# Optimization experiments

Measured on AMD Instinct MI355X. Metric: run time of the kernel, lower is better.

## Reference

```python
import jax, jax.numpy as jnp
import numpy as np

N_HOST, N_FLOW = 20000, 200000
D_HOST, D_FLOW, D_H, D_OUT, L = 64, 128, 256, 2, 2
E = 2000000


def _mean_agg(x_src, src, dst, num_dst):
    # SAGEConv default 'mean' neighbor aggregation: mean of source features per destination node.
    msg = x_src[src]                                            # [E, D]
    s = jax.ops.segment_sum(msg, dst, num_segments=num_dst)     # [num_dst, D]
    cnt = jax.ops.segment_sum(jnp.ones((src.shape[0],), x_src.dtype), dst, num_segments=num_dst)
    return s / jnp.maximum(cnt, 1.0)[:, None]


def setup_inputs() -> dict:
    key = jax.random.key(0)
    ks = jax.random.split(key, 20)
    s = 0.02
    inp = {
        'x_host': jax.random.normal(ks[0], (N_HOST, D_HOST), jnp.float32),
        'x_flow': jax.random.normal(ks[1], (N_FLOW, D_FLOW), jnp.float32),
        'eidx_hf_src': jax.random.randint(ks[2], (E,), 0, N_HOST, jnp.int32),
        'eidx_hf_dst': jax.random.randint(ks[3], (E,), 0, N_FLOW, jnp.int32),
        'eidx_fh_src': jax.random.randint(ks[4], (E,), 0, N_FLOW, jnp.int32),
        'eidx_fh_dst': jax.random.randint(ks[5], (E,), 0, N_HOST, jnp.int32),
        'host_proj_W': jax.random.normal(ks[6], (D_HOST, D_H), jnp.float32) * s,
        'host_proj_b': jnp.zeros((D_H,), jnp.float32),
        'flow_proj_W': jax.random.normal(ks[7], (D_FLOW, D_H), jnp.float32) * s,
        'flow_proj_b': jnp.zeros((D_H,), jnp.float32),
        # per-layer SAGEConv params: lin_l (neighbor agg, with bias), lin_r (root, no bias)
        'Wl_hf': jax.random.normal(ks[8], (L, D_H, D_H), jnp.float32) * s,
        'bl_hf': jnp.zeros((L, D_H), jnp.float32),
        'Wr_hf': jax.random.normal(ks[9], (L, D_H, D_H), jnp.float32) * s,
        'Wl_fh': jax.random.normal(ks[10], (L, D_H, D_H), jnp.float32) * s,
        'bl_fh': jnp.zeros((L, D_H), jnp.float32),
        'Wr_fh': jax.random.normal(ks[11], (L, D_H, D_H), jnp.float32) * s,
        'lin_W': jax.random.normal(ks[12], (D_H, D_OUT), jnp.float32) * s,
        'lin_b': jnp.zeros((D_OUT,), jnp.float32),
    }
    return inp


def reference(x_host, x_flow, eidx_hf_src, eidx_hf_dst, eidx_fh_src, eidx_fh_dst,
              host_proj_W, host_proj_b, flow_proj_W, flow_proj_b,
              Wl_hf, bl_hf, Wr_hf, Wl_fh, bl_fh, Wr_fh, lin_W, lin_b):
    n_host, n_flow = x_host.shape[0], x_flow.shape[0]
    h = jax.nn.relu(x_host @ host_proj_W + host_proj_b)   # [n_host, D_H]
    f = jax.nn.relu(x_flow @ flow_proj_W + flow_proj_b)   # [n_flow, D_H]
    for i in range(Wl_hf.shape[0]):
        # host -> flow SAGEConv
        agg_f = _mean_agg(h, eidx_hf_src, eidx_hf_dst, n_flow)
        new_f = agg_f @ Wl_hf[i] + bl_hf[i] + f @ Wr_hf[i]
        # flow -> host SAGEConv
        agg_h = _mean_agg(f, eidx_fh_src, eidx_fh_dst, n_host)
        new_h = agg_h @ Wl_fh[i] + bl_fh[i] + h @ Wr_fh[i]
        h = jax.nn.leaky_relu(new_h, 0.01)
        f = jax.nn.leaky_relu(new_f, 0.01)
    return f @ lin_W + lin_b  # logits for flow nodes [n_flow, D_OUT]
```

## Files before the change

### kernel.cpp

```cpp
#include <hip/hip_runtime.h>

#define NH    20000
#define NF    200000
#define DHOST 64
#define DFLOW 128
#define DHID  256
#define NE    2000000
#define NLAYER 2

typedef __attribute__((ext_vector_type(8))) short s16x8;
typedef __attribute__((ext_vector_type(4))) float f32x4;

__device__ __forceinline__ unsigned short f2bf(float x) {
    unsigned u = __builtin_bit_cast(unsigned, x);
    unsigned r = (u + 0x7fffu + ((u >> 16) & 1u)) >> 16;
    return (unsigned short)r;
}
__device__ __forceinline__ float bf2f(unsigned short h) {
    unsigned u = ((unsigned)h) << 16;
    return __builtin_bit_cast(float, u);
}

typedef const __attribute__((address_space(1))) unsigned int guint;
typedef __attribute__((address_space(3))) unsigned int luint;
__device__ __forceinline__ void gld16(const void* g, void* l) {
    __builtin_amdgcn_global_load_lds((guint*)g, (luint*)l, 16, 0, 0);
}

__device__ __forceinline__ void dq8(uint2 u, float s, float* a) {
#pragma unroll
    for (int j = 0; j < 4; ++j) {
        a[j]     += s * (float)((signed char)(u.x >> (8 * j)));
        a[4 + j] += s * (float)((signed char)(u.y >> (8 * j)));
    }
}

__global__ void zero_k(int* __restrict__ p, int n) {
    int i = blockIdx.x * 256 + threadIdx.x;
    if (i < n) p[i] = 0;
}

__global__ __launch_bounds__(256) void tpose_k(const float* __restrict__ W, unsigned short* __restrict__ Wt, int K) {
    __shared__ float T[32][33];
    int bx = blockIdx.x, by = blockIdx.y;
    const float* Wz = W + (size_t)blockIdx.z * K * 256;
    unsigned short* Wtz = Wt + (size_t)blockIdx.z * K * 256;
    int tx = threadIdx.x & 31, ty = threadIdx.x >> 5;
#pragma unroll
    for (int i = 0; i < 4; ++i) {
        int k = by * 32 + ty + i * 8;
        T[ty + i * 8][tx] = Wz[(size_t)k * 256 + bx * 32 + tx];
    }
    __syncthreads();
#pragma unroll
    for (int i = 0; i < 4; ++i) {
        int n = bx * 32 + ty + i * 8;
        Wtz[(size_t)n * K + by * 32 + tx] = f2bf(T[tx][ty + i * 8]);
    }
}

__global__ void scan1_k(const int* __restrict__ in, int n, int* __restrict__ out, int* __restrict__ bsum) {
    __shared__ int wsum[4];
    int t = threadIdx.x;
    int lane = t & 63, wave = t >> 6;
    int idx = blockIdx.x * 1024 + t * 4;
    int v[4]; int s = 0;
#pragma unroll
    for (int i = 0; i < 4; ++i) { v[i] = (idx + i < n) ? in[idx + i] : 0; s += v[i]; }
    int inc = s;
#pragma unroll
    for (int off = 1; off < 64; off <<= 1) { int u = __shfl_up(inc, off); if (lane >= off) inc += u; }
    if (lane == 63) wsum[wave] = inc;
    __syncthreads();
    int woff = 0;
    for (int w = 0; w < wave; ++w) woff += wsum[w];
    int ex = woff + inc - s;
#pragma unroll
    for (int i = 0; i < 4; ++i) { if (idx + i < n) out[idx + i] = ex; ex += v[i]; }
    if (t == 255) bsum[blockIdx.x] = woff + inc;
}

__global__ __launch_bounds__(256) void histAB(const int* __restrict__ dstA, const int* __restrict__ dstB,
                                              int E, int* __restrict__ gbhA, int* __restrict__ gbhB) {
    __shared__ int lh[391];
    const int g = blockIdx.y;
    const int* dst = g ? dstB : dstA;
    int* gbh = g ? gbhB : gbhA;
    const int SH = g ? 6 : 9;
    const int NBKT = g ? 313 : 391;
    for (int b = threadIdx.x; b < NBKT; b += 256) lh[b] = 0;
    __syncthreads();
#pragma unroll
    for (int k = 0; k < 8; ++k) {
        int i = blockIdx.x * 2048 + k * 256 + threadIdx.x;
        if (i < E) atomicAdd(&lh[dst[i] >> SH], 1);
    }
    __syncthreads();
    for (int b = threadIdx.x; b < NBKT; b += 256) if (lh[b]) atomicAdd(&gbh[b], lh[b]);
}

__global__ void initcur_k(int* __restrict__ bko, int* __restrict__ gcur, int nbkt, int E) {
    int i = blockIdx.x * 256 + threadIdx.x;
    if (i < nbkt) gcur[i] = bko[i];
    if (i == nbkt) bko[nbkt] = E;
}

__global__ __launch_bounds__(256) void binpassAB(const int* __restrict__ srcA, const int* __restrict__ dstA,
                                                 const int* __restrict__ srcB, const int* __restrict__ dstB,
                                                 int E, int* __restrict__ gcurA, int* __restrict__ gcurB,
                                                 int* __restrict__ pairsA, int* __restrict__ pairsB) {
    __shared__ int lh[391], resv[391], lc[391];
    const int g = blockIdx.y;
    const int* src = g ? srcB : srcA;
    const int* dst = g ? dstB : dstA;
    int* gcur = g ? gcurB : gcurA;
    int* pairs = g ? pairsB : pairsA;
    const int SH = g ? 6 : 9;
    const int NBKT = g ? 313 : 391;
    const int MSK = (1 << SH) - 1;
    const int tid = threadIdx.x;
    const int e0 = blockIdx.x * 8192;
    for (int b = tid; b < NBKT; b += 256) { lh[b] = 0; lc[b] = 0; }
    __syncthreads();
#pragma unroll 4
    for (int k = 0; k < 32; ++k) {
        int i = e0 + k * 256 + tid;
        if (i < E) atomicAdd(&lh[dst[i] >> SH], 1);
    }
    __syncthreads();
    for (int b = tid; b < NBKT; b += 256) if (lh[b]) resv[b] = atomicAdd(&gcur[b], lh[b]);
    __syncthreads();
#pragma unroll 4
    for (int k = 0; k < 32; ++k) {
        int i = e0 + k * 256 + tid;
        if (i < E) {
            int d = dst[i];
            int b = d >> SH;
            int p = resv[b] + atomicAdd(&lc[b], 1);
            pairs[p] = src[i] | ((d & MSK) << 18);
        }
    }
}

__global__ __launch_bounds__(256) void csrfinAB(const int* __restrict__ pairsA, const int* __restrict__ bkoA,
                                                const int* __restrict__ pairsB, const int* __restrict__ bkoB,
                                                int NBA, int E,
                                                int* __restrict__ rpA, int* __restrict__ colA,
                                                int* __restrict__ rpB, int* __restrict__ colB) {
    __shared__ int cnt[512], pos[512];
    __shared__ int wsum[4];
    const int tid = threadIdx.x;
    const bool isA = (int)blockIdx.x < NBA;
    const int b = isA ? blockIdx.x : blockIdx.x - NBA;
    const int SH = isA ? 9 : 6;
    const int NPB = isA ? 512 : 64;
    const int N = isA ? NF : NH;
    const int* pairs = isA ? pairsA : pairsB;
    const int* bko = isA ? bkoA : bkoB;
    int* rowptr = isA ? rpA : rpB;
    int* col = isA ? colA : colB;
    const int nb = b << SH;
    const int beg = bko[b], end = bko[b + 1];
    for (int i = tid; i < NPB; i += 256) cnt[i] = 0;
    __syncthreads();
    for (int i = beg + tid; i < end; i += 256) atomicAdd(&cnt[pairs[i] >> 18], 1);
    __syncthreads();
    int lane = tid & 63, wave = tid >> 6;
    if (NPB == 512) {
        int a = cnt[2 * tid], b2 = cnt[2 * tid + 1];
        int s = a + b2, incl = s;
#pragma unroll
        for (int off = 1; off < 64; off <<= 1) { int u = __shfl_up(incl, off); if (lane >= off) incl += u; }
        if (lane == 63) wsum[wave] = incl;
        __syncthreads();
        int woff = 0;
        for (int w = 0; w < wave; ++w) woff += wsum[w];
        int ex = woff + incl - s;
        pos[2 * tid] = ex; pos[2 * tid + 1] = ex + a;
    } else {
        if (tid < NPB) {
            int a = cnt[tid], incl = a;
#pragma unroll
            for (int off = 1; off < 64; off <<= 1) { int u = __shfl_up(incl, off); if (lane >= off) incl += u; }
            pos[tid] = incl - a;
        }
    }
    __syncthreads();
    for (int i = tid; i < NPB; i += 256) {
        int node = nb + i;
        if (node < N) rowptr[node] = beg + pos[i];
    }
    if (tid == 0 && end == E) rowptr[N] = E;
    __syncthreads();
    for (int i = beg + tid; i < end; i += 256) {
        int pk = pairs[i];
        int p = atomicAdd(&pos[pk >> 18], 1);
        col[beg + p] = pk & 0x3FFFF;
    }
}

__global__ __launch_bounds__(256) void agg8_q8(const signed char* __restrict__ qf,
                                               const float* __restrict__ scl,
                                               const int* __restrict__ rowptr,
                                               const int* __restrict__ col,
                                               unsigned short* __restrict__ outp, int n) {
    int w = (blockIdx.x << 2) + (threadIdx.x >> 6);
    if (w >= n) return;
    int lane = threadIdx.x & 63;
    int half = lane >> 5, l5 = lane & 31;
    int beg = rowptr[w], end = rowptr[w + 1];
    int T = end - beg;
    const signed char* base = qf + l5 * 8;
    float a0[8], a1[8], a2[8], a3[8], a4[8], a5[8], a6[8], a7[8];
#pragma unroll
    for (int j = 0; j < 8; ++j) {
        a0[j] = 0.f; a1[j] = 0.f; a2[j] = 0.f; a3[j] = 0.f;
        a4[j] = 0.f; a5[j] = 0.f; a6[j] = 0.f; a7[j] = 0.f;
    }
    int i = beg;
    int nb16 = T >> 4;
    {
        const int* cp = col + beg + half * 8;
        for (int k = 0; k < nb16; ++k) {
            int c0 = cp[k * 16 + 0], c1 = cp[k * 16 + 1], c2 = cp[k * 16 + 2], c3 = cp[k * 16 + 3];
            int c4 = cp[k * 16 + 4], c5 = cp[k * 16 + 5], c6 = cp[k * 16 + 6], c7 = cp[k * 16 + 7];
            uint2 u0 = *reinterpret_cast<const uint2*>(base + (size_t)c0 * DHID);
            uint2 u1 = *reinterpret_cast<const uint2*>(base + (size_t)c1 * DHID);
            uint2 u2 = *reinterpret_cast<const uint2*>(base + (size_t)c2 * DHID);
            uint2 u3 = *reinterpret_cast<const uint2*>(base + (size_t)c3 * DHID);
            uint2 u4 = *reinterpret_cast<const uint2*>(base + (size_t)c4 * DHID);
            uint2 u5 = *reinterpret_cast<const uint2*>(base + (size_t)c5 * DHID);
            uint2 u6 = *reinterpret_cast<const uint2*>(base + (size_t)c6 * DHID);
            uint2 u7 = *reinterpret_cast<const uint2*>(base + (size_t)c7 * DHID);
            float s0 = scl[c0], s1 = scl[c1], s2 = scl[c2], s3 = scl[c3];
            float s4 = scl[c4], s5 = scl[c5], s6 = scl[c6], s7 = scl[c7];
            dq8(u0, s0, a0); dq8(u1, s1, a1); dq8(u2, s2, a2); dq8(u3, s3, a3);
            dq8(u4, s4, a4); dq8(u5, s5, a5); dq8(u6, s6, a6); dq8(u7, s7, a7);
        }
    }
    i += nb16 * 16;
    if (end - i >= 8) {
        const int* cp = col + i + half * 4;
        int c0 = cp[0], c1 = cp[1], c2 = cp[2], c3 = cp[3];
        uint2 u0 = *reinterpret_cast<const uint2*>(base + (size_t)c0 * DHID);
        uint2 u1 = *reinterpret_cast<const uint2*>(base + (size_t)c1 * DHID);
        uint2 u2 = *reinterpret_cast<const uint2*>(base + (size_t)c2 * DHID);
        uint2 u3 = *reinterpret_cast<const uint2*>(base + (size_t)c3 * DHID);
        float s0 = scl[c0], s1 = scl[c1], s2 = scl[c2], s3 = scl[c3];
        dq8(u0, s0, a0); dq8(u1, s1, a1); dq8(u2, s2, a2); dq8(u3, s3, a3);
        i += 8;
    }
    for (int e = i + half; e < end; e += 2) {
        int c = col[e];
        uint2 u = *reinterpret_cast<const uint2*>(base + (size_t)c * DHID);
        dq8(u, scl[c], a0);
    }
    int deg = T > 0 ? T : 1;
    float inv = 1.0f / (float)deg;
    s16x8 o;
#pragma unroll
    for (int j = 0; j < 8; ++j) {
        float s = ((a0[j] + a1[j]) + (a2[j] + a3[j])) + ((a4[j] + a5[j]) + (a6[j] + a7[j]));
        s += __shfl_xor(s, 32);
        o[j] = (short)f2bf(s * inv);
    }
    if (half == 0)
        *reinterpret_cast<s16x8*>(outp + (size_t)w * DHID + l5 * 8) = o;
}

__device__ __forceinline__ unsigned swz(unsigned r, unsigned cb) {
    return r * 128u + (cb ^ ((r & 7u) << 4));
}

union SmU {
    struct { char A[64 * 128]; char B[256 * 128]; } st;
    unsigned short tile[64][256];
};

__device__ __forceinline__ void pass64(const unsigned short* A, const unsigned short* Wt,
                                       int m0, int M, int lane, int wave, int wr, int wc,
                                       f32x4 (&acc)[2][4], SmU& sm) {
    for (int k0 = 0; k0 < DHID; k0 += 64) {
        __syncthreads();
        {
            int r = wave * 8 + (lane >> 3);
            int gr = m0 + r; if (gr >= M) gr = M - 1;
            int gs = (lane & 7) ^ (r & 7);
            gld16(A + (size_t)gr * DHID + k0 + gs * 8, sm.st.A + wave * 1024);
        }
#pragma unroll
        for (int i = 0; i < 4; ++i) {
            int u = wave * 4 + i;
            int nn = u * 8 + (lane >> 3);
            int gs = (lane & 7) ^ (nn & 7);
            gld16(Wt + (size_t)nn * DHID + k0 + gs * 8, sm.st.B + u * 1024);
        }
        __syncthreads();
#pragma unroll
        for (int kk = 0; kk < 2; ++kk) {
            s16x8 ar[2], br[4];
            unsigned colb = (unsigned)(kk * 64 + (lane >> 4) * 16);
#pragma unroll
            for (int mf = 0; mf < 2; ++mf)
                ar[mf] = *reinterpret_cast<const s16x8*>(sm.st.A + swz((unsigned)(wr * 32 + mf * 16 + (lane & 15)), colb));
#pragma unroll
            for (int nf = 0; nf < 4; ++nf)
                br[nf] = *reinterpret_cast<const s16x8*>(sm.st.B + swz((unsigned)(wc * 64 + nf * 16 + (lane & 15)), colb));
#pragma unroll
            for (int mf = 0; mf < 2; ++mf)
#pragma unroll
                for (int nf = 0; nf < 4; ++nf)
                    acc[mf][nf] = __builtin_amdgcn_mfma_f32_16x16x32_bf16(ar[mf], br[nf], acc[mf][nf], 0, 0, 0);
        }
    }
}

template<int ACT, int POST>
__device__ __forceinline__ void epi64(f32x4 (&acc)[2][4], const float* bias, SmU& sm,
                                      int m0, int M, int lane, int wave, int wr, int wc,
                                      unsigned short* outp, signed char* q, float* scl) {
    const int col0 = wc * 64 + (lane & 15);
    float bc[4];
#pragma unroll
    for (int nf = 0; nf < 4; ++nf) bc[nf] = bias[col0 + nf * 16];
    if (POST == 0) {
#pragma unroll
        for (int mf = 0; mf < 2; ++mf) {
            int row = m0 + wr * 32 + mf * 16 + (lane >> 4) * 4;
#pragma unroll
            for (int j = 0; j < 4; ++j) {
                if (row + j < M) {
#pragma unroll
                    for (int nf = 0; nf < 4; ++nf) {
                        float v = acc[mf][nf][j] + bc[nf];
                        if (ACT == 1) v = fmaxf(v, 0.0f);
                        else if (ACT == 2) v = v > 0.0f ? v : 0.01f * v;
                        outp[(size_t)(row + j) * DHID + col0 + nf * 16] = f2bf(v);
                    }
                }
            }
        }
        return;
    }
    __syncthreads();
#pragma unroll
    for (int mf = 0; mf < 2; ++mf) {
        int rl = wr * 32 + mf * 16 + (lane >> 4) * 4;
#pragma unroll
        for (int j = 0; j < 4; ++j)
#pragma unroll
            for (int nf = 0; nf < 4; ++nf) {
                float v = acc[mf][nf][j] + bc[nf];
                if (ACT == 1) v = fmaxf(v, 0.0f);
                else if (ACT == 2) v = v > 0.0f ? v : 0.01f * v;
                sm.tile[rl + j][col0 + nf * 16] = f2bf(v);
            }
    }
    __syncthreads();
    const int half = lane >> 5, l5 = lane & 31;
    for (int t = 0; t < 4; ++t) {
        int local = wave * 8 + half * 4 + t;
        int node = m0 + local;
        s16x8 tr = *reinterpret_cast<const s16x8*>(&sm.tile[local][l5 * 8]);
        float v[8]; float m = 0.0f;
#pragma unroll
        for (int j = 0; j < 8; ++j) { v[j] = bf2f((unsigned short)tr[j]); m = fmaxf(m, fabsf(v[j])); }
#pragma unroll
        for (int off = 1; off < 32; off <<= 1) m = fmaxf(m, __shfl_xor(m, off));
        if (node < M) {
            if (POST == 1)
                *reinterpret_cast<s16x8*>(outp + (size_t)node * DHID + l5 * 8) = tr;
            float si = (m > 0.0f) ? 127.0f / m : 0.0f;
            if (l5 == 0) scl[node] = m * (1.0f / 127.0f);
            uint2 pk;
            pk.x = ((unsigned)((int)__builtin_rintf(v[0] * si) & 255))
                 | ((unsigned)((int)__builtin_rintf(v[1] * si) & 255) << 8)
                 | ((unsigned)((int)__builtin_rintf(v[2] * si) & 255) << 16)
                 | ((unsigned)((int)__builtin_rintf(v[3] * si) & 255) << 24);
            pk.y = ((unsigned)((int)__builtin_rintf(v[4] * si) & 255))
                 | ((unsigned)((int)__builtin_rintf(v[5] * si) & 255) << 8)
                 | ((unsigned)((int)__builtin_rintf(v[6] * si) & 255) << 16)
                 | ((unsigned)((int)__builtin_rintf(v[7] * si) & 255) << 24);
            *reinterpret_cast<uint2*>(q + (size_t)node * DHID + l5 * 8) = pk;
        }
    }
}

template<int ACT, int FUSE, int POST>
__global__ __launch_bounds__(512) void mgemm64(const unsigned short* A1, const unsigned short* W1t,
                                               const float* __restrict__ bias,
                                               const unsigned short* A2, const unsigned short* W2t,
                                               unsigned short* outp, signed char* q, float* scl, int M) {
    __shared__ SmU sm;
    const int tid = threadIdx.x;
    const int lane = tid & 63, wave = tid >> 6;
    const int wr = wave >> 2, wc = wave & 3;
    const int m0 = blockIdx.x * 64;
    f32x4 acc[2][4];
#pragma unroll
    for (int a = 0; a < 2; ++a)
#pragma unroll
        for (int b = 0; b < 4; ++b) acc[a][b] = (f32x4)0.0f;
    pass64(A1, W1t, m0, M, lane, wave, wr, wc, acc, sm);
    if (FUSE) pass64(A2, W2t, m0, M, lane, wave, wr, wc, acc, sm);
    epi64<ACT, POST>(acc, bias, sm, m0, M, lane, wave, wr, wc, outp, q, scl);
}

template<int K1, int ACT, int POST>
__global__ __launch_bounds__(512) void mgemm64_f32(const float* __restrict__ A1, const unsigned short* W1t,
                                                   const float* __restrict__ bias,
                                                   unsigned short* outp, signed char* q, float* scl, int M) {
    __shared__ SmU sm;
    const int tid = threadIdx.x;
    const int lane = tid & 63, wave = tid >> 6;
    const int wr = wave >> 2, wc = wave & 3;
    const int m0 = blockIdx.x * 64;
    f32x4 acc[2][4];
#pragma unroll
    for (int a = 0; a < 2; ++a)
#pragma unroll
        for (int b = 0; b < 4; ++b) acc[a][b] = (f32x4)0.0f;

    for (int k0 = 0; k0 < K1; k0 += 64) {
        __syncthreads();
        {
            int r = tid >> 3, gc = tid & 7;
            int gr = m0 + r; if (gr >= M) gr = M - 1;
            const float* src = A1 + (size_t)gr * K1 + k0 + gc * 8;
            float4 v0 = *reinterpret_cast<const float4*>(src);
            float4 v1 = *reinterpret_cast<const float4*>(src + 4);
            s16x8 o;
            o[0] = (short)f2bf(v0.x); o[1] = (short)f2bf(v0.y);
            o[2] = (short)f2bf(v0.z); o[3] = (short)f2bf(v0.w);
            o[4] = (short)f2bf(v1.x); o[5] = (short)f2bf(v1.y);
            o[6] = (short)f2bf(v1.z); o[7] = (short)f2bf(v1.w);
            *reinterpret_cast<s16x8*>(sm.st.A + swz((unsigned)r, (unsigned)(gc * 16))) = o;
        }
#pragma unroll
        for (int i = 0; i < 4; ++i) {
            int u = wave * 4 + i;
            int nn = u * 8 + (lane >> 3);
            int gs = (lane & 7) ^ (nn & 7);
            gld16(W1t + (size_t)nn * K1 + k0 + gs * 8, sm.st.B + u * 1024);
        }
        __syncthreads();
#pragma unroll
        for (int kk = 0; kk < 2; ++kk) {
            s16x8 ar[2], br[4];
            unsigned colb = (unsigned)(kk * 64 + (lane >> 4) * 16);
#pragma unroll
            for (int mf = 0; mf < 2; ++mf)
                ar[mf] = *reinterpret_cast<const s16x8*>(sm.st.A + swz((unsigned)(wr * 32 + mf * 16 + (lane & 15)), colb));
#pragma unroll
            for (int nf = 0; nf < 4; ++nf)
                br[nf] = *reinterpret_cast<const s16x8*>(sm.st.B + swz((unsigned)(wc * 64 + nf * 16 + (lane & 15)), colb));
#pragma unroll
            for (int mf = 0; mf < 2; ++mf)
#pragma unroll
                for (int nf = 0; nf < 4; ++nf)
                    acc[mf][nf] = __builtin_amdgcn_mfma_f32_16x16x32_bf16(ar[mf], br[nf], acc[mf][nf], 0, 0, 0);
        }
    }
    epi64<ACT, POST>(acc, bias, sm, m0, M, lane, wave, wr, wc, outp, q, scl);
}

template<int QOUT>
__global__ __launch_bounds__(512) void mgemm_faq(const unsigned short* Fin, const unsigned short* Wrt,
                                                 const float* __restrict__ bias,
                                                 const signed char* __restrict__ Hq,
                                                 const float* __restrict__ sclH,
                                                 const int* __restrict__ rowptr,
                                                 const int* __restrict__ colv,
                                                 unsigned short* Fout,
                                                 signed char* __restrict__ Fq,
                                                 float* __restrict__ sclF, int M) {
    __shared__ SmU sm;
    const int tid = threadIdx.x;
    const int lane = tid & 63, wave = tid >> 6;
    const int wr = wave >> 2, wc = wave & 3;
    const int m0 = blockIdx.x * 64;
    f32x4 acc[2][4];
#pragma unroll
    for (int a = 0; a < 2; ++a)
#pragma unroll
        for (int b = 0; b < 4; ++b) acc[a][b] = (f32x4)0.0f;

    pass64(Fin, Wrt, m0, M, lane, wave, wr, wc, acc, sm);
    __syncthreads();

    const int col0 = wc * 64 + (lane & 15);
    float bc[4];
#pragma unroll
    for (int nf = 0; nf < 4; ++nf) bc[nf] = bias[col0 + nf * 16];
#pragma unroll
    for (int mf = 0; mf < 2; ++mf) {
        int rl = wr * 32 + mf * 16 + (lane >> 4) * 4;
#pragma unroll
        for (int j = 0; j < 4; ++j)
#pragma unroll
            for (int nf = 0; nf < 4; ++nf)
                sm.tile[rl + j][col0 + nf * 16] = f2bf(acc[mf][nf][j] + bc[nf]);
    }
    __syncthreads();

    const int half = lane >> 5, l5 = lane & 31;
    const signed char* base = Hq + l5 * 8;
    for (int t = 0; t < 8; ++t) {
        int local = wave * 8 + t;
        int node = m0 + local;
        if (node >= M) break;
        int beg = rowptr[node], end = rowptr[node + 1];
        int T = end - beg;
        int nb8 = T >> 3;
        float a0[8], a1[8], a2[8], a3[8];
#pragma unroll
        for (int j = 0; j < 8; ++j) { a0[j] = 0.f; a1[j] = 0.f; a2[j] = 0.f; a3[j] = 0.f; }
        const int* cp = colv + beg + half * 4;
        for (int k = 0; k < nb8; ++k) {
            int c0 = cp[k * 8 + 0], c1 = cp[k * 8 + 1], c2 = cp[k * 8 + 2], c3 = cp[k * 8 + 3];
            uint2 u0 = *reinterpret_cast<const uint2*>(base + (size_t)c0 * DHID);
            uint2 u1 = *reinterpret_cast<const uint2*>(base + (size_t)c1 * DHID);
            uint2 u2 = *reinterpret_cast<const uint2*>(base + (size_t)c2 * DHID);
            uint2 u3 = *reinterpret_cast<const uint2*>(base + (size_t)c3 * DHID);
            float s0 = sclH[c0], s1 = sclH[c1], s2 = sclH[c2], s3 = sclH[c3];
            dq8(u0, s0, a0); dq8(u1, s1, a1); dq8(u2, s2, a2); dq8(u3, s3, a3);
        }
        for (int i = beg + nb8 * 8 + half; i < end; i += 2) {
            int c = colv[i];
            uint2 u = *reinterpret_cast<const uint2*>(base + (size_t)c * DHID);
            dq8(u, sclH[c], a0);
        }
        float inv = 1.0f / (float)(T > 0 ? T : 1);
        s16x8 tr = *reinterpret_cast<const s16x8*>(&sm.tile[local][l5 * 8]);
        float v[8]; float m = 0.0f;
        s16x8 o;
#pragma unroll
        for (int j = 0; j < 8; ++j) {
            float s = (a0[j] + a1[j]) + (a2[j] + a3[j]);
            s += __shfl_xor(s, 32);
            float x = bf2f((unsigned short)tr[j]) + s * inv;
            x = x > 0.0f ? x : 0.01f * x;
            v[j] = x; o[j] = (short)f2bf(x);
            m = fmaxf(m, fabsf(x));
        }
        if (half == 0)
            *reinterpret_cast<s16x8*>(Fout + (size_t)node * DHID + l5 * 8) = o;
        if (QOUT) {
#pragma unroll
            for (int off = 1; off < 32; off <<= 1) m = fmaxf(m, __shfl_xor(m, off));
            float si = (m > 0.0f) ? 127.0f / m : 0.0f;
            if (half == 0 && l5 == 0) sclF[node] = m * (1.0f / 127.0f);
            if (half == 0) {
                uint2 pk;
                pk.x = ((unsigned)((int)__builtin_rintf(v[0] * si) & 255))
                     | ((unsigned)((int)__builtin_rintf(v[1] * si) & 255) << 8)
                     | ((unsigned)((int)__builtin_rintf(v[2] * si) & 255) << 16)
                     | ((unsigned)((int)__builtin_rintf(v[3] * si) & 255) << 24);
                pk.y = ((unsigned)((int)__builtin_rintf(v[4] * si) & 255))
                     | ((unsigned)((int)__builtin_rintf(v[5] * si) & 255) << 8)
                     | ((unsigned)((int)__builtin_rintf(v[6] * si) & 255) << 16)
                     | ((unsigned)((int)__builtin_rintf(v[7] * si) & 255) << 24);
                *reinterpret_cast<uint2*>(Fq + (size_t)node * DHID + l5 * 8) = pk;
            }
        }
    }
}

__global__ __launch_bounds__(256) void head_k(const unsigned short* __restrict__ f, const float* __restrict__ W,
                                              const float* __restrict__ b, float* __restrict__ outp, int M) {
    int row = blockIdx.x * 4 + (threadIdx.x >> 6);
    if (row >= M) return;
    int lane = threadIdx.x & 63;
    ushort4 v = *reinterpret_cast<const ushort4*>(f + (size_t)row * DHID + lane * 4);
    float4 w0 = *reinterpret_cast<const float4*>(W + lane * 8);
    float4 w1 = *reinterpret_cast<const float4*>(W + lane * 8 + 4);
    float a0 = bf2f(v.x) * w0.x + bf2f(v.y) * w0.z + bf2f(v.z) * w1.x + bf2f(v.w) * w1.z;
    float a1 = bf2f(v.x) * w0.y + bf2f(v.y) * w0.w + bf2f(v.z) * w1.y + bf2f(v.w) * w1.w;
#pragma unroll
    for (int off = 32; off > 0; off >>= 1) {
        a0 += __shfl_down(a0, off);
        a1 += __shfl_down(a1, off);
    }
    if (lane == 0) {
        outp[(size_t)row * 2 + 0] = a0 + b[0];
        outp[(size_t)row * 2 + 1] = a1 + b[1];
    }
}

extern "C" void kernel_launch(void* const* d_in, const int* in_sizes, int n_in,
                              void* d_out, int out_size, void* d_ws, size_t ws_size,
                              hipStream_t stream) {
    const float* x_host  = (const float*)d_in[0];
    const float* x_flow  = (const float*)d_in[1];
    const int*   hf_src  = (const int*)d_in[2];
    const int*   hf_dst  = (const int*)d_in[3];
    const int*   fh_src  = (const int*)d_in[4];
    const int*   fh_dst  = (const int*)d_in[5];
    const float* host_W  = (const float*)d_in[6];
    const float* host_b  = (const float*)d_in[7];
    const float* flow_W  = (const float*)d_in[8];
    const float* flow_b  = (const float*)d_in[9];
    const float* Wl_hf   = (const float*)d_in[10];
    const float* bl_hf   = (const float*)d_in[11];
    const float* Wr_hf   = (const float*)d_in[12];
    const float* Wl_fh   = (const float*)d_in[13];
    const float* bl_fh   = (const float*)d_in[14];
    const float* Wr_fh   = (const float*)d_in[15];
    const float* lin_W   = (const float*)d_in[16];
    const float* lin_b   = (const float*)d_in[17];

    char* ws = (char*)d_ws;
    size_t off = 0;
    auto alloc = [&](size_t bytes) -> char* {
        char* p = ws + off;
        off += (bytes + 255) & ~(size_t)255;
        return p;
    };
    typedef unsigned short u16;
    u16* F     = (u16*)alloc((size_t)NF * DHID * 2);
    u16* H     = (u16*)alloc((size_t)NH * DHID * 2);
    u16* AggH  = (u16*)alloc((size_t)NH * DHID * 2);
    signed char* Fq = (signed char*)alloc((size_t)NF * DHID);
    signed char* Hq = (signed char*)alloc((size_t)NH * DHID);
    float* sclF = (float*)alloc((size_t)NF * 4);
    float* sclH = (float*)alloc((size_t)NH * 4);
    u16* hostWt = (u16*)alloc((size_t)DHID * DHOST * 2);
    u16* flowWt = (u16*)alloc((size_t)DHID * DFLOW * 2);
    u16* WlhfT  = (u16*)alloc((size_t)NLAYER * DHID * DHID * 2);
    u16* WrhfT  = (u16*)alloc((size_t)NLAYER * DHID * DHID * 2);
    u16* WlfhT  = (u16*)alloc((size_t)NLAYER * DHID * DHID * 2);
    u16* WrfhT  = (u16*)alloc((size_t)NLAYER * DHID * DHID * 2);
    float* zbias = (float*)alloc(DHID * 4);
    int* rp_hf  = (int*)alloc((size_t)(NF + 1) * 4);
    int* col_hf = (int*)alloc((size_t)NE * 4);
    int* rp_fh  = (int*)alloc((size_t)(NH + 1) * 4);
    int* col_fh = (int*)alloc((size_t)NE * 4);
    int* pairsA = (int*)alloc((size_t)NE * 4);
    int* pairsB = (int*)alloc((size_t)NE * 4);
    int* gbh2   = (int*)alloc(1024 * 4);
    int* bkoA   = (int*)alloc(513 * 4);
    int* bkoB   = (int*)alloc(513 * 4);
    int* gcurA  = (int*)alloc(512 * 4);
    int* gcurB  = (int*)alloc(512 * 4);
    int* junk   = (int*)alloc(4);
    int* gbhA = gbh2, *gbhB = gbh2 + 512;

    const int NBKT_HF = (NF + 511) / 512;
    const int NBKT_FH = (NH + 63) / 64;

    zero_k<<<4, 256, 0, stream>>>(gbh2, 1024);
    histAB<<<dim3((NE + 2047) / 2048, 2), 256, 0, stream>>>(hf_dst, fh_dst, NE, gbhA, gbhB);
    scan1_k<<<1, 256, 0, stream>>>(gbhA, NBKT_HF, bkoA, junk);
    scan1_k<<<1, 256, 0, stream>>>(gbhB, NBKT_FH, bkoB, junk);
    initcur_k<<<2, 256, 0, stream>>>(bkoA, gcurA, NBKT_HF, NE);
    initcur_k<<<2, 256, 0, stream>>>(bkoB, gcurB, NBKT_FH, NE);
    binpassAB<<<dim3((NE + 8191) / 8192, 2), 256, 0, stream>>>(hf_src, hf_dst, fh_src, fh_dst, NE,
                                                               gcurA, gcurB, pairsA, pairsB);
    csrfinAB<<<NBKT_HF + NBKT_FH, 256, 0, stream>>>(pairsA, bkoA, pairsB, bkoB, NBKT_HF, NE,
                                                    rp_hf, col_hf, rp_fh, col_fh);

    zero_k<<<1, 256, 0, stream>>>((int*)zbias, DHID);
    tpose_k<<<dim3(8, DHOST / 32, 1), 256, 0, stream>>>(host_W, hostWt, DHOST);
    tpose_k<<<dim3(8, DFLOW / 32, 1), 256, 0, stream>>>(flow_W, flowWt, DFLOW);
    tpose_k<<<dim3(8, 8, NLAYER), 256, 0, stream>>>(Wl_hf, WlhfT, DHID);
    tpose_k<<<dim3(8, 8, NLAYER), 256, 0, stream>>>(Wr_hf, WrhfT, DHID);
    tpose_k<<<dim3(8, 8, NLAYER), 256, 0, stream>>>(Wl_fh, WlfhT, DHID);
    tpose_k<<<dim3(8, 8, NLAYER), 256, 0, stream>>>(Wr_fh, WrfhT, DHID);

    mgemm64_f32<DHOST, 1, 0><<<(NH + 63) / 64, 512, 0, stream>>>(x_host, hostWt, host_b, H, nullptr, nullptr, NH);
    mgemm64_f32<DFLOW, 1, 1><<<(NF + 63) / 64, 512, 0, stream>>>(x_flow, flowWt, flow_b, F, Fq, sclF, NF);

    for (int i = 0; i < NLAYER; ++i) {
        const u16* wl_hf = WlhfT + (size_t)i * DHID * DHID;
        const u16* wr_hf = WrhfT + (size_t)i * DHID * DHID;
        const u16* wl_fh = WlfhT + (size_t)i * DHID * DHID;
        const u16* wr_fh = WrfhT + (size_t)i * DHID * DHID;
        const float* b_hf = bl_hf + (size_t)i * DHID;
        const float* b_fh = bl_fh + (size_t)i * DHID;

        mgemm64<0, 0, 2><<<(NH + 63) / 64, 512, 0, stream>>>(H, wl_hf, zbias, H, wl_hf,
                                                             nullptr, Hq, sclH, NH);

        agg8_q8<<<(NH + 3) / 4, 256, 0, stream>>>(Fq, sclF, rp_fh, col_fh, AggH, NH);

        if (i + 1 < NLAYER)
            mgemm_faq<1><<<(NF + 63) / 64, 512, 0, stream>>>(F, wr_hf, b_hf, Hq, sclH,
                                                             rp_hf, col_hf, F, Fq, sclF, NF);
        else
            mgemm_faq<0><<<(NF + 63) / 64, 512, 0, stream>>>(F, wr_hf, b_hf, Hq, sclH,
                                                             rp_hf, col_hf, F, Fq, sclF, NF);

        mgemm64<2, 1, 0><<<(NH + 63) / 64, 512, 0, stream>>>(AggH, wl_fh, b_fh, H, wr_fh,
                                                             H, nullptr, nullptr, NH);
    }

    head_k<<<(NF + 3) / 4, 256, 0, stream>>>(F, lin_W, lin_b, (float*)d_out, NF);
}
```

Measured before the change: 889.7 us.

## Drop dead final-layer host update and fuse output head into last flow GEMM

Unrolls the two-layer loop so the last layer skips work that never reaches the output. That removes the flow-to-host aggregation, the host GEMM and the int8 quantization of flow features that only fed the next layer's host aggregation. The final linear head is fused into the last mgemm_faq epilogue as a per-row dot product with a wave reduction. This avoids writing the final bf16 flow features and re-reading them in a separate head kernel. In exchange the layer count is hard-coded to two and the fused epilogue needs some extra registers and shuffles.

```diff
diff --git a/kernel.cpp b/kernel.cpp
--- a/kernel.cpp
+++ b/kernel.cpp
@@ -6,7 +6,6 @@
 #define DFLOW 128
 #define DHID  256
 #define NE    2000000
-#define NLAYER 2
 
 typedef __attribute__((ext_vector_type(8))) short s16x8;
 typedef __attribute__((ext_vector_type(4))) float f32x4;
@@ -464,7 +463,7 @@
     epi64<ACT, POST>(acc, bias, sm, m0, M, lane, wave, wr, wc, outp, q, scl);
 }
 
-template<int QOUT>
+template<int HEAD>
 __global__ __launch_bounds__(512) void mgemm_faq(const unsigned short* Fin, const unsigned short* Wrt,
                                                  const float* __restrict__ bias,
                                                  const signed char* __restrict__ Hq,
@@ -472,8 +471,9 @@
                                                  const int* __restrict__ rowptr,
                                                  const int* __restrict__ colv,
                                                  unsigned short* Fout,
-                                                 signed char* __restrict__ Fq,
-                                                 float* __restrict__ sclF, int M) {
+                                                 const float* __restrict__ linW,
+                                                 const float* __restrict__ linb,
+                                                 float* __restrict__ outHead, int M) {
     __shared__ SmU sm;
     const int tid = threadIdx.x;
     const int lane = tid & 63, wave = tid >> 6;
@@ -505,6 +505,15 @@
 
     const int half = lane >> 5, l5 = lane & 31;
     const signed char* base = Hq + l5 * 8;
+    float w0[8], w1[8], hb0 = 0.0f, hb1 = 0.0f;
+    if (HEAD) {
+#pragma unroll
+        for (int j = 0; j < 8; ++j) {
+            w0[j] = linW[(l5 * 8 + j) * 2 + 0];
+            w1[j] = linW[(l5 * 8 + j) * 2 + 1];
+        }
+        hb0 = linb[0]; hb1 = linb[1];
+    }
     for (int t = 0; t < 8; ++t) {
         int local = wave * 8 + t;
         int node = m0 + local;
@@ -532,7 +541,7 @@
         }
         float inv = 1.0f / (float)(T > 0 ? T : 1);
         s16x8 tr = *reinterpret_cast<const s16x8*>(&sm.tile[local][l5 * 8]);
-        float v[8]; float m = 0.0f;
+        float v[8];
         s16x8 o;
 #pragma unroll
         for (int j = 0; j < 8; ++j) {
@@ -541,49 +550,24 @@
             float x = bf2f((unsigned short)tr[j]) + s * inv;
             x = x > 0.0f ? x : 0.01f * x;
             v[j] = x; o[j] = (short)f2bf(x);
-            m = fmaxf(m, fabsf(x));
-        }
-        if (half == 0)
-            *reinterpret_cast<s16x8*>(Fout + (size_t)node * DHID + l5 * 8) = o;
-        if (QOUT) {
-#pragma unroll
-            for (int off = 1; off < 32; off <<= 1) m = fmaxf(m, __shfl_xor(m, off));
-            float si = (m > 0.0f) ? 127.0f / m : 0.0f;
-            if (half == 0 && l5 == 0) sclF[node] = m * (1.0f / 127.0f);
-            if (half == 0) {
-                uint2 pk;
-                pk.x = ((unsigned)((int)__builtin_rintf(v[0] * si) & 255))
-                     | ((unsigned)((int)__builtin_rintf(v[1] * si) & 255) << 8)
-                     | ((unsigned)((int)__builtin_rintf(v[2] * si) & 255) << 16)
-                     | ((unsigned)((int)__builtin_rintf(v[3] * si) & 255) << 24);
-                pk.y = ((unsigned)((int)__builtin_rintf(v[4] * si) & 255))
-                     | ((unsigned)((int)__builtin_rintf(v[5] * si) & 255) << 8)
-                     | ((unsigned)((int)__builtin_rintf(v[6] * si) & 255) << 16)
-                     | ((unsigned)((int)__builtin_rintf(v[7] * si) & 255) << 24);
-                *reinterpret_cast<uint2*>(Fq + (size_t)node * DHID + l5 * 8) = pk;
+        }
+        if (HEAD) {
+            float p0 = 0.0f, p1 = 0.0f;
+#pragma unroll
+            for (int j = 0; j < 8; ++j) { p0 += v[j] * w0[j]; p1 += v[j] * w1[j]; }
+#pragma unroll
+            for (int off = 1; off < 32; off <<= 1) {
+                p0 += __shfl_xor(p0, off);
+                p1 += __shfl_xor(p1, off);
             }
-        }
-    }
-}
-
-__global__ __launch_bounds__(256) void head_k(const unsigned short* __restrict__ f, const float* __restrict__ W,
-                                              const float* __restrict__ b, float* __restrict__ outp, int M) {
-    int row = blockIdx.x * 4 + (threadIdx.x >> 6);
-    if (row >= M) return;
-    int lane = threadIdx.x & 63;
-    ushort4 v = *reinterpret_cast<const ushort4*>(f + (size_t)row * DHID + lane * 4);
-    float4 w0 = *reinterpret_cast<const float4*>(W + lane * 8);
-    float4 w1 = *reinterpret_cast<const float4*>(W + lane * 8 + 4);
-    float a0 = bf2f(v.x) * w0.x + bf2f(v.y) * w0.z + bf2f(v.z) * w1.x + bf2f(v.w) * w1.z;
-    float a1 = bf2f(v.x) * w0.y + bf2f(v.y) * w0.w + bf2f(v.z) * w1.y + bf2f(v.w) * w1.w;
-#pragma unroll
-    for (int off = 32; off > 0; off >>= 1) {
-        a0 += __shfl_down(a0, off);
-        a1 += __shfl_down(a1, off);
-    }
-    if (lane == 0) {
-        outp[(size_t)row * 2 + 0] = a0 + b[0];
-        outp[(size_t)row * 2 + 1] = a1 + b[1];
+            if (lane == 0) {
+                outHead[(size_t)node * 2 + 0] = p0 + hb0;
+                outHead[(size_t)node * 2 + 1] = p1 + hb1;
+            }
+        } else {
+            if (half == 0)
+                *reinterpret_cast<s16x8*>(Fout + (size_t)node * DHID + l5 * 8) = o;
+        }
     }
 }
 
@@ -626,10 +610,10 @@
     float* sclH = (float*)alloc((size_t)NH * 4);
     u16* hostWt = (u16*)alloc((size_t)DHID * DHOST * 2);
     u16* flowWt = (u16*)alloc((size_t)DHID * DFLOW * 2);
-    u16* WlhfT  = (u16*)alloc((size_t)NLAYER * DHID * DHID * 2);
-    u16* WrhfT  = (u16*)alloc((size_t)NLAYER * DHID * DHID * 2);
-    u16* WlfhT  = (u16*)alloc((size_t)NLAYER * DHID * DHID * 2);
-    u16* WrfhT  = (u16*)alloc((size_t)NLAYER * DHID * DHID * 2);
+    u16* WlhfT  = (u16*)alloc((size_t)2 * DHID * DHID * 2);
+    u16* WrhfT  = (u16*)alloc((size_t)2 * DHID * DHID * 2);
+    u16* WlfhT  = (u16*)alloc((size_t)2 * DHID * DHID * 2);
+    u16* WrfhT  = (u16*)alloc((size_t)2 * DHID * DHID * 2);
     float* zbias = (float*)alloc(DHID * 4);
     int* rp_hf  = (int*)alloc((size_t)(NF + 1) * 4);
     int* col_hf = (int*)alloc((size_t)NE * 4);
@@ -662,37 +646,39 @@
     zero_k<<<1, 256, 0, stream>>>((int*)zbias, DHID);
     tpose_k<<<dim3(8, DHOST / 32, 1), 256, 0, stream>>>(host_W, hostWt, DHOST);
     tpose_k<<<dim3(8, DFLOW / 32, 1), 256, 0, stream>>>(flow_W, flowWt, DFLOW);
-    tpose_k<<<dim3(8, 8, NLAYER), 256, 0, stream>>>(Wl_hf, WlhfT, DHID);
-    tpose_k<<<dim3(8, 8, NLAYER), 256, 0, stream>>>(Wr_hf, WrhfT, DHID);
-    tpose_k<<<dim3(8, 8, NLAYER), 256, 0, stream>>>(Wl_fh, WlfhT, DHID);
-    tpose_k<<<dim3(8, 8, NLAYER), 256, 0, stream>>>(Wr_fh, WrfhT, DHID);
+    tpose_k<<<dim3(8, 8, 2), 256, 0, stream>>>(Wl_hf, WlhfT, DHID);
+    tpose_k<<<dim3(8, 8, 2), 256, 0, stream>>>(Wr_hf, WrhfT, DHID);
+    tpose_k<<<dim3(8, 8, 2), 256, 0, stream>>>(Wl_fh, WlfhT, DHID);
+    tpose_k<<<dim3(8, 8, 2), 256, 0, stream>>>(Wr_fh, WrfhT, DHID);
 
     mgemm64_f32<DHOST, 1, 0><<<(NH + 63) / 64, 512, 0, stream>>>(x_host, hostWt, host_b, H, nullptr, nullptr, NH);
     mgemm64_f32<DFLOW, 1, 1><<<(NF + 63) / 64, 512, 0, stream>>>(x_flow, flowWt, flow_b, F, Fq, sclF, NF);
 
-    for (int i = 0; i < NLAYER; ++i) {
-        const u16* wl_hf = WlhfT + (size_t)i * DHID * DHID;
-        const u16* wr_hf = WrhfT + (size_t)i * DHID * DHID;
-        const u16* wl_fh = WlfhT + (size_t)i * DHID * DHID;
-        const u16* wr_fh = WrfhT + (size_t)i * DHID * DHID;
-        const float* b_hf = bl_hf + (size_t)i * DHID;
-        const float* b_fh = bl_fh + (size_t)i * DHID;
+    {
+        const u16* wl_hf = WlhfT;
+        const u16* wr_hf = WrhfT;
+        const u16* wl_fh = WlfhT;
+        const u16* wr_fh = WrfhT;
 
         mgemm64<0, 0, 2><<<(NH + 63) / 64, 512, 0, stream>>>(H, wl_hf, zbias, H, wl_hf,
                                                              nullptr, Hq, sclH, NH);
-
         agg8_q8<<<(NH + 3) / 4, 256, 0, stream>>>(Fq, sclF, rp_fh, col_fh, AggH, NH);
-
-        if (i + 1 < NLAYER)
-            mgemm_faq<1><<<(NF + 63) / 64, 512, 0, stream>>>(F, wr_hf, b_hf, Hq, sclH,
-                                                             rp_hf, col_hf, F, Fq, sclF, NF);
-        else
-            mgemm_faq<0><<<(NF + 63) / 64, 512, 0, stream>>>(F, wr_hf, b_hf, Hq, sclH,
-                                                             rp_hf, col_hf, F, Fq, sclF, NF);
-
-        mgemm64<2, 1, 0><<<(NH + 63) / 64, 512, 0, stream>>>(AggH, wl_fh, b_fh, H, wr_fh,
+        mgemm_faq<0><<<(NF + 63) / 64, 512, 0, stream>>>(F, wr_hf, bl_hf, Hq, sclH,
+                                                         rp_hf, col_hf, F,
+                                                         nullptr, nullptr, nullptr, NF);
+        mgemm64<2, 1, 0><<<(NH + 63) / 64, 512, 0, stream>>>(AggH, wl_fh, bl_fh, H, wr_fh,
                                                              H, nullptr, nullptr, NH);
     }
 
-    head_k<<<(NF + 3) / 4, 256, 0, stream>>>(F, lin_W, lin_b, (float*)d_out, NF);
-}
+    {
+        const u16* wl_hf = WlhfT + (size_t)DHID * DHID;
+        const u16* wr_hf = WrhfT + (size_t)DHID * DHID;
+        const float* b_hf = bl_hf + DHID;
+
+        mgemm64<0, 0, 2><<<(NH + 63) / 64, 512, 0, stream>>>(H, wl_hf, zbias, H, wl_hf,
+                                                             nullptr, Hq, sclH, NH);
+        mgemm_faq<1><<<(NF + 63) / 64, 512, 0, stream>>>(F, wr_hf, b_hf, Hq, sclH,
+                                                         rp_hf, col_hf, nullptr,
+                                                         lin_W, lin_b, (float*)d_out, NF);
+    }
+}
```

Measured after the change: 736.4 us, median of 2. -17.2%, faster.
